# Optimization experiments

Hardware: AMD Instinct MI355X
Metric: run time of the kernel (lower is better)

Reference implementation:

```python
import jax, jax.numpy as jnp
import numpy as np

D_MODEL = 1024
N_HEADS = 16
HEAD_DIM = D_MODEL // N_HEADS  # d_keys = d_values = 64
EPS = 1e-10


def setup_inputs() -> dict:
    key = jax.random.key(0)
    ks = jax.random.split(key, 11)
    N, L, S = 4, 4096, 4096
    inp = {
        'queries': jax.random.normal(ks[0], (N, L, D_MODEL), jnp.float32),
        'keys': jax.random.normal(ks[1], (N, S, D_MODEL), jnp.float32),
        'values': jax.random.normal(ks[2], (N, S, D_MODEL), jnp.float32),
        # Dense layer params (glorot-ish scale)
        'Wq': jax.random.normal(ks[3], (D_MODEL, D_MODEL), jnp.float32) / np.sqrt(D_MODEL),
        'bq': jnp.zeros((D_MODEL,), jnp.float32),
        'Wk': jax.random.normal(ks[4], (D_MODEL, D_MODEL), jnp.float32) / np.sqrt(D_MODEL),
        'bk': jnp.zeros((D_MODEL,), jnp.float32),
        'Wv': jax.random.normal(ks[5], (D_MODEL, D_MODEL), jnp.float32) / np.sqrt(D_MODEL),
        'bv': jnp.zeros((D_MODEL,), jnp.float32),
        'Wo': jax.random.normal(ks[6], (D_MODEL, D_MODEL), jnp.float32) / np.sqrt(D_MODEL),
        'bo': jnp.zeros((D_MODEL,), jnp.float32),
    }
    return inp


def _feat(x):
    # elu(x) + 1 feature map (strictly positive)
    return jax.nn.elu(x) + 1.0


def reference(queries, keys, values, Wq, bq, Wk, bk, Wv, bv, Wo, bo):
    N, L, _ = queries.shape
    S = keys.shape[1]
    H, Dh = N_HEADS, HEAD_DIM
    # projections -> [n, l, h, d]
    Q = (queries @ Wq + bq).reshape(N, L, H, Dh)
    K = (keys @ Wk + bk).reshape(N, S, H, Dh)
    V = (values @ Wv + bv).reshape(N, S, H, Dh)
    Q_lin = _feat(Q)
    K_lin = _feat(K)
    # normalizer Z: [n, l, h]
    K_sum = K_lin.sum(axis=1)  # [n, h, d]
    Z = 1.0 / (jnp.einsum('nlhd,nhd->nlh', Q_lin, K_sum) + EPS)
    # KV outer-product accumulation: [n, h, m, d]
    KV = jnp.einsum('nshd,nshm->nhmd', K_lin, V)
    # attention output: [n, l, h, m]
    V_lin = jnp.einsum('nlhd,nhmd,nlh->nlhm', Q_lin, KV, Z)
    new_values = V_lin.reshape(N, L, H * Dh)
    return new_values @ Wo + bo
```

## Files before the change

kernel.cpp:

```cpp
#include <hip/hip_runtime.h>
#include <hip/hip_bf16.h>
#include <stdint.h>

#define D_MODEL 1024
#define NHEADS  16
#define DH      64
#define NBATCH  4
#define SEQLEN  4096
#define MROWS   (NBATCH*SEQLEN)
#define EPSV    1e-10f

typedef __hip_bfloat16 bf16;
typedef unsigned short ushort_t;
typedef __attribute__((ext_vector_type(8))) short short8;
typedef __attribute__((ext_vector_type(4))) float f32x4;

struct __align__(8) bf16x4s { bf16 a, b, c, d; };

__device__ __forceinline__ void async_copy16(void* lds, const void* g) {
  __builtin_amdgcn_global_load_lds(
      (const __attribute__((address_space(1))) unsigned int*)(uintptr_t)g,
      (__attribute__((address_space(3))) unsigned int*)(uintptr_t)lds,
      16, 0, 0);
}

__device__ __forceinline__ short f2bf_bits(float v) {
  bf16 b = __float2bfloat16(v);
  short s; __builtin_memcpy(&s, &b, 2); return s;
}
__device__ __forceinline__ float bfbits_to_f(ushort_t u) {
  return __uint_as_float(((unsigned int)u) << 16);
}

__global__ __launch_bounds__(256)
void cvt_bf16(const float* __restrict__ s, bf16* __restrict__ d) {
  const int i = blockIdx.x * 256 + threadIdx.x;
  const f32x4 v = ((const f32x4*)s)[i];
  bf16x4s o;
  o.a = __float2bfloat16(v[0]);
  o.b = __float2bfloat16(v[1]);
  o.c = __float2bfloat16(v[2]);
  o.d = __float2bfloat16(v[3]);
  ((bf16x4s*)d)[i] = o;
}

__global__ void transpose4(const float* __restrict__ s0, const float* __restrict__ s1,
                           const float* __restrict__ s2, const float* __restrict__ s3,
                           bf16* __restrict__ d0, bf16* __restrict__ d1,
                           bf16* __restrict__ d2, bf16* __restrict__ d3) {
  const float* s; bf16* d;
  switch (blockIdx.z) {
    case 0: s = s0; d = d0; break;
    case 1: s = s1; d = d1; break;
    case 2: s = s2; d = d2; break;
    default: s = s3; d = d3; break;
  }
  __shared__ float tile[32][33];
  int x = blockIdx.x*32 + threadIdx.x;
  int y = blockIdx.y*32 + threadIdx.y;
  tile[threadIdx.y][threadIdx.x] = s[(size_t)y*D_MODEL + x];
  __syncthreads();
  int xo = blockIdx.y*32 + threadIdx.x;
  int yo = blockIdx.x*32 + threadIdx.y;
  d[(size_t)yo*D_MODEL + xo] = __float2bfloat16(tile[threadIdx.x][threadIdx.y]);
}

__device__ __forceinline__ void storeC(float* p, float v) { *p = v; }
__device__ __forceinline__ void storeC(bf16*  p, float v) { *p = __float2bfloat16(v); }

template<int ACT, typename CT>
__global__ __launch_bounds__(256, 2)
void gemm_bias_act(const bf16* __restrict__ A, const bf16* __restrict__ BT,
                   const float* __restrict__ bias, CT* __restrict__ C,
                   int M, int N, int K) {
  __shared__ __align__(16) short Asm[128*32];
  __shared__ __align__(16) short Bsm[256*32];
  const int tid  = threadIdx.x;
  const int wave = tid >> 6;
  const int lane = tid & 63;
  const int m0 = blockIdx.y * 128;
  const int n0 = blockIdx.x * 256;
  const int wr = wave >> 1, wc = wave & 1;
  const int srow = tid >> 2;
  const int scol = (tid & 3) * 8;
  const int fr   = lane & 15;
  const int quad = lane >> 4;

  f32x4 acc[4][8] = {};

  for (int k0 = 0; k0 < K; k0 += 32) {
    __syncthreads();
    #pragma unroll
    for (int r = 0; r < 2; ++r) {
      const int row = r*64 + srow;
      async_copy16(&Asm[row*32 + scol], A + (size_t)(m0+row)*K + k0 + scol);
    }
    #pragma unroll
    for (int r = 0; r < 4; ++r) {
      const int row = r*64 + srow;
      async_copy16(&Bsm[row*32 + scol], BT + (size_t)(n0+row)*K + k0 + scol);
    }
    __syncthreads();
    short8 afr[4], bfr[8];
    #pragma unroll
    for (int i = 0; i < 4; ++i)
      afr[i] = *(const short8*)&Asm[(wr*64 + i*16 + fr)*32 + quad*8];
    #pragma unroll
    for (int j = 0; j < 8; ++j)
      bfr[j] = *(const short8*)&Bsm[(wc*128 + j*16 + fr)*32 + quad*8];
    #pragma unroll
    for (int i = 0; i < 4; ++i)
      #pragma unroll
      for (int j = 0; j < 8; ++j)
        acc[i][j] = __builtin_amdgcn_mfma_f32_16x16x32_bf16(afr[i], bfr[j], acc[i][j], 0, 0, 0);
  }

  #pragma unroll
  for (int j = 0; j < 8; ++j) {
    const int gn = n0 + wc*128 + j*16 + fr;
    const float bv = bias[gn];
    #pragma unroll
    for (int i = 0; i < 4; ++i) {
      const int gm = m0 + wr*64 + i*16 + quad*4;
      #pragma unroll
      for (int r2 = 0; r2 < 4; ++r2) {
        float v = acc[i][j][r2] + bv;
        if (ACT) v = (v > 0.f) ? (v + 1.f) : __expf(v);
        storeC(&C[(size_t)(gm + r2)*N + gn], v);
      }
    }
  }
}

#define KV_SPLIT 16
__global__ __launch_bounds__(256)
void kv_kernel(const bf16* __restrict__ Kl, const bf16* __restrict__ V,
               float* __restrict__ KVp, float* __restrict__ Ksp) {
  const int b  = blockIdx.x;
  const int sp = b & (KV_SPLIT-1);
  const int nh = b >> 4;
  const int h = nh & (NHEADS-1), n = nh >> 4;
  const int tid = threadIdx.x;
  const int wave = tid >> 6, lane = tid & 63;
  const int fr = lane & 15, quad = lane >> 4;
  const int d = lane;

  __shared__ __align__(16) short Kt[64*64];
  __shared__ __align__(16) short Vt[64*64];
  __shared__ float Ksl[4][64];

  const ushort_t* Kg = (const ushort_t*)Kl;
  const ushort_t* Vg = (const ushort_t*)V;

  f32x4 acc[4] = {};
  float ksacc = 0.f;
  const int s_base = sp * (SEQLEN / KV_SPLIT);

  for (int c0 = 0; c0 < 256; c0 += 64) {
    __syncthreads();
    #pragma unroll
    for (int i = 0; i < 2; ++i) {
      const int s8 = wave*2 + i;
      const size_t gbase = ((size_t)(n*SEQLEN + s_base + c0 + s8*8))*D_MODEL + h*DH + d;
      short8 pk, pv;
      #pragma unroll
      for (int e = 0; e < 8; ++e) {
        const ushort_t ku = Kg[gbase + (size_t)e*D_MODEL];
        const ushort_t vu = Vg[gbase + (size_t)e*D_MODEL];
        pk[e] = (short)ku;
        pv[e] = (short)vu;
        ksacc += bfbits_to_f(ku);
      }
      const int wofs = d*64 + ((s8 ^ (d & 7)) << 3);
      *(short8*)&Kt[wofs] = pk;
      *(short8*)&Vt[wofs] = pv;
    }
    __syncthreads();
    #pragma unroll
    for (int k0 = 0; k0 < 2; ++k0) {
      const int s8a = k0*4 + quad;
      const int arow = wave*16 + fr;
      const short8 afr = *(const short8*)&Vt[arow*64 + ((s8a ^ (arow & 7)) << 3)];
      #pragma unroll
      for (int j = 0; j < 4; ++j) {
        const int brow = j*16 + fr;
        const short8 bfr = *(const short8*)&Kt[brow*64 + ((s8a ^ (brow & 7)) << 3)];
        acc[j] = __builtin_amdgcn_mfma_f32_16x16x32_bf16(afr, bfr, acc[j], 0, 0, 0);
      }
    }
  }

  Ksl[wave][d] = ksacc;
  __syncthreads();
  if (tid < 64)
    Ksp[b*64 + tid] = Ksl[0][tid] + Ksl[1][tid] + Ksl[2][tid] + Ksl[3][tid];

  float* outp = KVp + (size_t)b*4096;
  #pragma unroll
  for (int j = 0; j < 4; ++j)
    #pragma unroll
    for (int r = 0; r < 4; ++r)
      outp[(wave*16 + quad*4 + r)*64 + j*16 + fr] = acc[j][r];
}

__global__ __launch_bounds__(256)
void kv_reduce(const float* __restrict__ KVp, const float* __restrict__ Ksp,
               float* __restrict__ KV, float* __restrict__ Ksum) {
  const int c  = blockIdx.x;
  const int nh = blockIdx.y;
  const int e = c*1024 + threadIdx.x*4;
  f32x4 s = {};
  #pragma unroll
  for (int sp = 0; sp < KV_SPLIT; ++sp)
    s += *(const f32x4*)(KVp + ((size_t)(nh*KV_SPLIT + sp))*4096 + e);
  *(f32x4*)(KV + (size_t)nh*4096 + e) = s;
  if (c == 0 && threadIdx.x < 64) {
    float ks = 0.f;
    #pragma unroll
    for (int sp = 0; sp < KV_SPLIT; ++sp)
      ks += Ksp[(nh*KV_SPLIT + sp)*64 + threadIdx.x];
    Ksum[nh*64 + threadIdx.x] = ks;
  }
}

__device__ __forceinline__ int bswz(int row, int d) {
  return row*64 + ((((d >> 3) ^ (row & 7)) << 3) | (d & 7));
}

__global__ __launch_bounds__(256)
void vlin_kernel(const bf16* __restrict__ Ql, const float* __restrict__ KV,
                 const float* __restrict__ Ksum, bf16* __restrict__ Vl) {
  const int lc = blockIdx.x;
  const int nh = blockIdx.y;
  const int h = nh & (NHEADS-1), n = nh >> 4;
  const int tid = threadIdx.x, wave = tid >> 6, lane = tid & 63;
  const int fr = lane & 15, quad = lane >> 4;

  __shared__ __align__(16) short Bs[144*64];
  __shared__ float Zs[128];

  const float* kvp = KV + (size_t)nh*DH*DH;
  for (int i = tid; i < DH*DH; i += 256) {
    const int m = i >> 6, d = i & 63;
    const float v = kvp[i];
    const short hi = f2bf_bits(v);
    bf16 hb; __builtin_memcpy(&hb, &hi, 2);
    const short lo = f2bf_bits(v - __bfloat162float(hb));
    Bs[bswz(m, d)]      = hi;
    Bs[bswz(64 + m, d)] = lo;
  }
  if (tid < 64) {
    const float v = Ksum[nh*DH + tid];
    const short hi = f2bf_bits(v);
    bf16 hb; __builtin_memcpy(&hb, &hi, 2);
    const short lo = f2bf_bits(v - __bfloat162float(hb));
    Bs[bswz(128, tid)] = hi;
    Bs[bswz(129, tid)] = lo;
  }
  for (int i = tid; i < 14*64; i += 256)
    Bs[(130 + (i >> 6))*64 + (i & 63)] = 0;
  __syncthreads();

  const int l0 = lc * 128;
  const size_t qbase = ((size_t)(n*SEQLEN) + l0)*D_MODEL + h*DH;
  short8 afr[2][2];
  #pragma unroll
  for (int i = 0; i < 2; ++i)
    #pragma unroll
    for (int ks = 0; ks < 2; ++ks)
      afr[i][ks] = *(const short8*)(Ql + qbase +
                     (size_t)(wave*32 + i*16 + fr)*D_MODEL + ks*32 + quad*8);

  f32x4 acc[2][9] = {};
  #pragma unroll
  for (int ks = 0; ks < 2; ++ks) {
    #pragma unroll
    for (int j = 0; j < 9; ++j) {
      const int brow = j*16 + fr;
      const short8 bfr = *(const short8*)&Bs[brow*64 +
                            (((ks*4 + quad) ^ (fr & 7)) << 3)];
      #pragma unroll
      for (int i = 0; i < 2; ++i)
        acc[i][j] = __builtin_amdgcn_mfma_f32_16x16x32_bf16(afr[i][ks], bfr, acc[i][j], 0, 0, 0);
    }
  }

  #pragma unroll
  for (int i = 0; i < 2; ++i) {
    #pragma unroll
    for (int r2 = 0; r2 < 4; ++r2) {
      const float v = acc[i][8][r2];
      const float vp = v + __shfl_xor(v, 1, 64);
      if (fr == 0) Zs[wave*32 + i*16 + quad*4 + r2] = 1.0f / (vp + EPSV);
    }
  }
  __syncthreads();

  #pragma unroll
  for (int i = 0; i < 2; ++i) {
    #pragma unroll
    for (int r2 = 0; r2 < 4; ++r2) {
      const int rloc = wave*32 + i*16 + quad*4 + r2;
      const float z = Zs[rloc];
      #pragma unroll
      for (int j = 0; j < 4; ++j) {
        const float num = acc[i][j][r2] + acc[i][4 + j][r2];
        Vl[qbase + (size_t)rloc*D_MODEL + j*16 + fr] = __float2bfloat16(num * z);
      }
    }
  }
}

extern "C" void kernel_launch(void* const* d_in, const int* in_sizes, int n_in,
                              void* d_out, int out_size, void* d_ws, size_t ws_size,
                              hipStream_t stream) {
  const float* q  = (const float*)d_in[0];
  const float* k  = (const float*)d_in[1];
  const float* v  = (const float*)d_in[2];
  const float* Wq = (const float*)d_in[3];
  const float* bq = (const float*)d_in[4];
  const float* Wk = (const float*)d_in[5];
  const float* bk = (const float*)d_in[6];
  const float* Wv = (const float*)d_in[7];
  const float* bv = (const float*)d_in[8];
  const float* Wo = (const float*)d_in[9];
  const float* bo = (const float*)d_in[10];
  float* out = (float*)d_out;

  bf16* WqT = (bf16*)d_ws;
  bf16* WkT = WqT + (size_t)D_MODEL*D_MODEL;
  bf16* WvT = WkT + (size_t)D_MODEL*D_MODEL;
  bf16* WoT = WvT + (size_t)D_MODEL*D_MODEL;
  bf16* Xb  = WoT + (size_t)D_MODEL*D_MODEL;
  bf16* Ql  = Xb  + (size_t)MROWS*D_MODEL;
  bf16* Kl  = Ql  + (size_t)MROWS*D_MODEL;
  bf16* Vb  = Kl  + (size_t)MROWS*D_MODEL;
  bf16* Vl  = Kl;
  float* KV = (float*)(Vb + (size_t)MROWS*D_MODEL);
  float* Ks = KV + (size_t)NBATCH*NHEADS*DH*DH;
  float* KVp = (float*)Xb;
  float* Ksp = KVp + (size_t)NBATCH*NHEADS*KV_SPLIT*DH*DH;

  transpose4<<<dim3(32,32,4), dim3(32,32,1), 0, stream>>>(Wq,Wk,Wv,Wo, WqT,WkT,WvT,WoT);

  const int nconv4 = MROWS*D_MODEL/4;
  dim3 gb(256), gg(D_MODEL/256, MROWS/128);

  cvt_bf16<<<nconv4/256, 256, 0, stream>>>(q, Xb);
  gemm_bias_act<1,bf16><<<gg, gb, 0, stream>>>(Xb, WqT, bq, Ql, MROWS, D_MODEL, D_MODEL);
  cvt_bf16<<<nconv4/256, 256, 0, stream>>>(k, Xb);
  gemm_bias_act<1,bf16><<<gg, gb, 0, stream>>>(Xb, WkT, bk, Kl, MROWS, D_MODEL, D_MODEL);
  cvt_bf16<<<nconv4/256, 256, 0, stream>>>(v, Xb);
  gemm_bias_act<0,bf16><<<gg, gb, 0, stream>>>(Xb, WvT, bv, Vb, MROWS, D_MODEL, D_MODEL);

  kv_kernel<<<dim3(NBATCH*NHEADS*KV_SPLIT), dim3(256), 0, stream>>>(Kl, Vb, KVp, Ksp);
  kv_reduce<<<dim3(4, NBATCH*NHEADS), dim3(256), 0, stream>>>(KVp, Ksp, KV, Ks);
  vlin_kernel<<<dim3(SEQLEN/128, NBATCH*NHEADS), dim3(256), 0, stream>>>(Ql, KV, Ks, Vl);

  gemm_bias_act<0,float><<<gg, gb, 0, stream>>>(Vl, WoT, bo, out, MROWS, D_MODEL, D_MODEL);
}
```

Baseline: 487.4 us.

## Rewrite projection GEMM as 256x256 tile, 8-wave, double-buffered ping-pong pipeline

Replaces the single-buffered 128x256 GEMM with a 256x256 tile run by 512 threads. It uses double-buffered 64-wide K stages in LDS, XOR-swizzled LDS addressing, and explicit barrier/vmcnt scheduling that interleaves async global-to-LDS copies with MFMA phases. It also remaps block IDs so neighbouring workgroups share tiles. The aim is to hide global load latency and remove the two syncthreads stalls per K step, at the cost of 128KB of LDS per block and fragile hand-written wait counts. The vlin kernel's shared array is only renamed.

```diff
diff --git a/kernel.cpp b/kernel.cpp
--- a/kernel.cpp
+++ b/kernel.cpp
@@ -69,67 +69,135 @@
 __device__ __forceinline__ void storeC(bf16*  p, float v) { *p = __float2bfloat16(v); }
 
 template<int ACT, typename CT>
-__global__ __launch_bounds__(256, 2)
+__global__ __launch_bounds__(512, 2)
 void gemm_bias_act(const bf16* __restrict__ A, const bf16* __restrict__ BT,
                    const float* __restrict__ bias, CT* __restrict__ C,
                    int M, int N, int K) {
-  __shared__ __align__(16) short Asm[128*32];
-  __shared__ __align__(16) short Bsm[256*32];
+  __shared__ __align__(16) short As[2*256*64];
+  __shared__ __align__(16) short Bs[2*256*64];
   const int tid  = threadIdx.x;
-  const int wave = tid >> 6;
+  const int w    = tid >> 6;
   const int lane = tid & 63;
-  const int m0 = blockIdx.y * 128;
-  const int n0 = blockIdx.x * 256;
-  const int wr = wave >> 1, wc = wave & 1;
-  const int srow = tid >> 2;
-  const int scol = (tid & 3) * 8;
   const int fr   = lane & 15;
   const int quad = lane >> 4;
-
-  f32x4 acc[4][8] = {};
-
-  for (int k0 = 0; k0 < K; k0 += 32) {
-    __syncthreads();
-    #pragma unroll
-    for (int r = 0; r < 2; ++r) {
-      const int row = r*64 + srow;
-      async_copy16(&Asm[row*32 + scol], A + (size_t)(m0+row)*K + k0 + scol);
-    }
-    #pragma unroll
-    for (int r = 0; r < 4; ++r) {
-      const int row = r*64 + srow;
-      async_copy16(&Bsm[row*32 + scol], BT + (size_t)(n0+row)*K + k0 + scol);
-    }
-    __syncthreads();
-    short8 afr[4], bfr[8];
-    #pragma unroll
-    for (int i = 0; i < 4; ++i)
-      afr[i] = *(const short8*)&Asm[(wr*64 + i*16 + fr)*32 + quad*8];
-    #pragma unroll
-    for (int j = 0; j < 8; ++j)
-      bfr[j] = *(const short8*)&Bsm[(wc*128 + j*16 + fr)*32 + quad*8];
-    #pragma unroll
-    for (int i = 0; i < 4; ++i)
-      #pragma unroll
-      for (int j = 0; j < 8; ++j)
-        acc[i][j] = __builtin_amdgcn_mfma_f32_16x16x32_bf16(afr[i], bfr[j], acc[i][j], 0, 0, 0);
-  }
-
-  #pragma unroll
-  for (int j = 0; j < 8; ++j) {
-    const int gn = n0 + wc*128 + j*16 + fr;
+  const int la   = lane >> 3;
+  const int gp   = lane & 7;
+  const int gl   = gp ^ la;
+
+  const int nbx = N >> 8;
+  const int nwg = (M >> 8) * nbx;
+  int fid = blockIdx.y * nbx + blockIdx.x;
+  fid = (fid & 7) * (nwg >> 3) + (fid >> 3);
+  const int m0 = (fid / nbx) * 256;
+  const int n0 = (fid % nbx) * 256;
+  const int wr = w >> 2, wc = w & 3;
+
+  f32x4 acc[8][4] = {};
+  const int nit = K >> 7;
+
+#define STAGE_A(d, h, kt) do {                                              \
+    const int kb_ = (kt)*64;                                                \
+    _Pragma("unroll") for (int r_ = 0; r_ < 2; ++r_) {                      \
+      const int row_ = r_*128 + (h)*64 + w*8 + la;                          \
+      async_copy16(&As[((d)*256 + row_)*64 + gp*8],                         \
+                   A + (size_t)(m0 + row_)*K + kb_ + gl*8);                 \
+    } } while (0)
+#define STAGE_B(d, h, kt) do {                                              \
+    const int kb_ = (kt)*64;                                                \
+    _Pragma("unroll") for (int r_ = 0; r_ < 2; ++r_) {                      \
+      const int row_ = (r_*2 + (w>>2))*64 + (h)*32 + (w&3)*8 + la;          \
+      async_copy16(&Bs[((d)*256 + row_)*64 + gp*8],                         \
+                   BT + (size_t)(n0 + row_)*K + kb_ + gl*8);                \
+    } } while (0)
+
+#define VM4  asm volatile("s_waitcnt vmcnt(4)" ::: "memory")
+#define VM0  asm volatile("s_waitcnt vmcnt(0)" ::: "memory")
+#define NOWAIT ((void)0)
+#define NOSTAGE ((void)0)
+
+#define PHASE(d, qm, qn, STAGE_STMT, END_WAIT) {                            \
+    short8 af_[4][2], bf_[2][2];                                            \
+    const int pg0_ = (quad ^ (fr & 7)) * 8;                                 \
+    const int pg1_ = ((4 + quad) ^ (fr & 7)) * 8;                           \
+    const int ab_ = (d)*16384 + (wr*128 + fr)*64;                           \
+    _Pragma("unroll") for (int m2_ = 0; m2_ < 4; ++m2_) {                   \
+      af_[m2_][0] = *(const short8*)&As[ab_ + ((qm)*4 + m2_)*1024 + pg0_];  \
+      af_[m2_][1] = *(const short8*)&As[ab_ + ((qm)*4 + m2_)*1024 + pg1_];  \
+    }                                                                       \
+    const int bb_ = (d)*16384 + (wc*64 + fr)*64;                            \
+    _Pragma("unroll") for (int n2_ = 0; n2_ < 2; ++n2_) {                   \
+      bf_[n2_][0] = *(const short8*)&Bs[bb_ + ((qn)*2 + n2_)*1024 + pg0_];  \
+      bf_[n2_][1] = *(const short8*)&Bs[bb_ + ((qn)*2 + n2_)*1024 + pg1_];  \
+    }                                                                       \
+    STAGE_STMT;                                                             \
+    asm volatile("s_barrier" ::: "memory");                                 \
+    asm volatile("s_waitcnt lgkmcnt(0)" ::: "memory");                      \
+    __builtin_amdgcn_s_setprio(1);                                          \
+    _Pragma("unroll") for (int m2_ = 0; m2_ < 4; ++m2_)                     \
+    _Pragma("unroll") for (int n2_ = 0; n2_ < 2; ++n2_)                     \
+    _Pragma("unroll") for (int ks_ = 0; ks_ < 2; ++ks_)                     \
+      acc[(qm)*4 + m2_][(qn)*2 + n2_] =                                     \
+        __builtin_amdgcn_mfma_f32_16x16x32_bf16(af_[m2_][ks_], bf_[n2_][ks_],\
+            acc[(qm)*4 + m2_][(qn)*2 + n2_], 0, 0, 0);                      \
+    __builtin_amdgcn_s_setprio(0);                                          \
+    END_WAIT;                                                               \
+    asm volatile("s_barrier" ::: "memory");                                 \
+  }
+
+  STAGE_A(0, 0, 0);
+  STAGE_A(0, 1, 0);
+  STAGE_B(0, 0, 0);
+  STAGE_B(0, 1, 0);
+  STAGE_A(1, 0, 1);
+  STAGE_B(1, 0, 1);
+  VM4;
+  asm volatile("s_barrier" ::: "memory");
+
+  for (int i = 0; i < nit - 1; ++i) {
+    const int ti = 2 * i;
+    PHASE(0, 0, 0, STAGE_A(1, 1, ti + 1), NOWAIT)
+    PHASE(0, 0, 1, STAGE_B(1, 1, ti + 1), NOWAIT)
+    PHASE(0, 1, 0, STAGE_A(0, 0, ti + 2), NOWAIT)
+    PHASE(0, 1, 1, STAGE_B(0, 0, ti + 2), VM4)
+    PHASE(1, 0, 0, STAGE_A(0, 1, ti + 2), NOWAIT)
+    PHASE(1, 0, 1, STAGE_B(0, 1, ti + 2), NOWAIT)
+    PHASE(1, 1, 0, STAGE_A(1, 0, ti + 3), NOWAIT)
+    PHASE(1, 1, 1, STAGE_B(1, 0, ti + 3), VM4)
+  }
+  {
+    const int ti = 2 * (nit - 1);
+    PHASE(0, 0, 0, STAGE_A(1, 1, ti + 1), NOWAIT)
+    PHASE(0, 0, 1, STAGE_B(1, 1, ti + 1), NOWAIT)
+    PHASE(0, 1, 0, NOSTAGE, NOWAIT)
+    PHASE(0, 1, 1, NOSTAGE, VM0)
+    PHASE(1, 0, 0, NOSTAGE, NOWAIT)
+    PHASE(1, 0, 1, NOSTAGE, NOWAIT)
+    PHASE(1, 1, 0, NOSTAGE, NOWAIT)
+    PHASE(1, 1, 1, NOSTAGE, NOWAIT)
+  }
+
+  #pragma unroll
+  for (int nf = 0; nf < 4; ++nf) {
+    const int gn = n0 + wc*64 + nf*16 + fr;
     const float bv = bias[gn];
     #pragma unroll
-    for (int i = 0; i < 4; ++i) {
-      const int gm = m0 + wr*64 + i*16 + quad*4;
+    for (int mf = 0; mf < 8; ++mf) {
+      const int gm = m0 + wr*128 + mf*16 + quad*4;
       #pragma unroll
       for (int r2 = 0; r2 < 4; ++r2) {
-        float v = acc[i][j][r2] + bv;
+        float v = acc[mf][nf][r2] + bv;
         if (ACT) v = (v > 0.f) ? (v + 1.f) : __expf(v);
         storeC(&C[(size_t)(gm + r2)*N + gn], v);
       }
     }
   }
+#undef STAGE_A
+#undef STAGE_B
+#undef PHASE
+#undef VM4
+#undef VM0
+#undef NOWAIT
+#undef NOSTAGE
 }
 
 #define KV_SPLIT 16
@@ -236,7 +304,7 @@
   const int tid = threadIdx.x, wave = tid >> 6, lane = tid & 63;
   const int fr = lane & 15, quad = lane >> 4;
 
-  __shared__ __align__(16) short Bs[144*64];
+  __shared__ __align__(16) short Bs2[144*64];
   __shared__ float Zs[128];
 
   const float* kvp = KV + (size_t)nh*DH*DH;
@@ -246,19 +314,19 @@
     const short hi = f2bf_bits(v);
     bf16 hb; __builtin_memcpy(&hb, &hi, 2);
     const short lo = f2bf_bits(v - __bfloat162float(hb));
-    Bs[bswz(m, d)]      = hi;
-    Bs[bswz(64 + m, d)] = lo;
+    Bs2[bswz(m, d)]      = hi;
+    Bs2[bswz(64 + m, d)] = lo;
   }
   if (tid < 64) {
     const float v = Ksum[nh*DH + tid];
     const short hi = f2bf_bits(v);
     bf16 hb; __builtin_memcpy(&hb, &hi, 2);
     const short lo = f2bf_bits(v - __bfloat162float(hb));
-    Bs[bswz(128, tid)] = hi;
-    Bs[bswz(129, tid)] = lo;
+    Bs2[bswz(128, tid)] = hi;
+    Bs2[bswz(129, tid)] = lo;
   }
   for (int i = tid; i < 14*64; i += 256)
-    Bs[(130 + (i >> 6))*64 + (i & 63)] = 0;
+    Bs2[(130 + (i >> 6))*64 + (i & 63)] = 0;
   __syncthreads();
 
   const int l0 = lc * 128;
@@ -277,7 +345,7 @@
     #pragma unroll
     for (int j = 0; j < 9; ++j) {
       const int brow = j*16 + fr;
-      const short8 bfr = *(const short8*)&Bs[brow*64 +
+      const short8 bfr = *(const short8*)&Bs2[brow*64 +
                             (((ks*4 + quad) ^ (fr & 7)) << 3)];
       #pragma unroll
       for (int i = 0; i < 2; ++i)
@@ -344,7 +412,7 @@
   transpose4<<<dim3(32,32,4), dim3(32,32,1), 0, stream>>>(Wq,Wk,Wv,Wo, WqT,WkT,WvT,WoT);
 
   const int nconv4 = MROWS*D_MODEL/4;
-  dim3 gb(256), gg(D_MODEL/256, MROWS/128);
+  dim3 gb(512), gg(D_MODEL/256, MROWS/256);
 
   cvt_bf16<<<nconv4/256, 256, 0, stream>>>(q, Xb);
   gemm_bias_act<1,bf16><<<gg, gb, 0, stream>>>(Xb, WqT, bq, Ql, MROWS, D_MODEL, D_MODEL);
```

Result: faster. 466.9 us (-4.2%).
